# Optimization experiments

Hardware: AMD Instinct MI355X
Metric: run time of the kernel (lower is better)

The kernel has to match this reference:

```python
import jax, jax.numpy as jnp
import numpy as np

B, T, C, H = 2, 2048, 2048, 16
HD = C // H  # head dim = 128
ROPE_BASE = 10000.0


def apply_rope(x):
    # x: [B, T, H, HD]; interleaved-pair rotation as in torchtune RoPE
    t = x.shape[1]
    half = x.shape[-1] // 2
    theta = 1.0 / (ROPE_BASE ** (jnp.arange(0, HD, 2, dtype=jnp.float32) / HD))  # [HD/2]
    ang = jnp.arange(t, dtype=jnp.float32)[:, None] * theta[None, :]  # [T, HD/2]
    cos = jnp.cos(ang)[None, :, None, :]  # [1, T, 1, HD/2]
    sin = jnp.sin(ang)[None, :, None, :]
    xs = x.reshape(*x.shape[:-1], half, 2)  # [B,T,H,HD/2,2]
    x0, x1 = xs[..., 0], xs[..., 1]
    out = jnp.stack([x0 * cos - x1 * sin, x1 * cos + x0 * sin], axis=-1)
    return out.reshape(x.shape)


def setup_inputs() -> dict:
    key = jax.random.key(0)
    k1, k2, k3 = jax.random.split(key, 3)
    x = jax.random.normal(k1, (B, T, C), dtype=jnp.float32)
    attn_mask = jnp.tril(jnp.ones((T, T), dtype=bool))[None, None]  # causal [1,1,T,T]
    W_attn = jax.random.normal(k2, (3 * C, C), dtype=jnp.float32) * (C ** -0.5)
    W_proj = jax.random.normal(k3, (C, C), dtype=jnp.float32) * (C ** -0.5)
    return {"x": x, "attn_mask": attn_mask, "W_attn": W_attn, "W_proj": W_proj}


def reference(x, attn_mask, W_attn, W_proj):
    b, t, c = x.shape
    qkv = x @ W_attn.T  # [B,T,3C]
    q, k, v = jnp.split(qkv, 3, axis=-1)
    q = apply_rope(q.reshape(b, t, H, HD)).transpose(0, 2, 1, 3)  # [B,H,T,HD]
    k = apply_rope(k.reshape(b, t, H, HD)).transpose(0, 2, 1, 3)
    v = v.reshape(b, t, H, HD).transpose(0, 2, 1, 3)
    scale = 1.0 / jnp.sqrt(jnp.float32(HD))
    scores = jnp.einsum("bhqd,bhkd->bhqk", q, k) * scale
    scores = jnp.where(attn_mask, scores, jnp.finfo(scores.dtype).min)
    probs = jax.nn.softmax(scores, axis=-1)
    y = jnp.einsum("bhqk,bhkd->bhqd", probs, v)  # [B,H,T,HD]
    y = y.transpose(0, 2, 1, 3).reshape(b, t, c)
    return y @ W_proj.T
```

## Files before the change

### kernel.cpp

```cpp
#include <hip/hip_runtime.h>
#include <hip/hip_bf16.h>
#include <math.h>

typedef unsigned short u16;
typedef unsigned int   u32;
typedef __attribute__((ext_vector_type(8)))  short bf16x8;
typedef __attribute__((ext_vector_type(4)))  float f32x4;
typedef __attribute__((ext_vector_type(16))) float f32x16;

#define B_  2
#define T_  2048
#define C_  2048
#define H_  16
#define HD_ 128
#define M_  4096
#define N3C 6144

__device__ __forceinline__ float bf2f_lo(u32 u) { return __uint_as_float(u << 16); }
__device__ __forceinline__ float bf2f_hi(u32 u) { return __uint_as_float(u & 0xffff0000u); }

__device__ __forceinline__ u16 f2bf(float f) {
    u32 u = __float_as_uint(f);
    return (u16)((u + 0x7fffu + ((u >> 16) & 1u)) >> 16);
}
__device__ __forceinline__ u32 pack2(float a, float b) {
    return (u32)f2bf(a) | ((u32)f2bf(b) << 16);
}
__device__ __forceinline__ void store1(float* p, float v) { *p = v; }
__device__ __forceinline__ void store1(__hip_bfloat16* p, float v) { *(u16*)p = f2bf(v); }

__device__ __forceinline__ void gload16(const void* g, void* l) {
    __builtin_amdgcn_global_load_lds((__attribute__((address_space(1))) void*)g,
                                     (__attribute__((address_space(3))) void*)l, 16, 0, 0);
}

__global__ __launch_bounds__(256) void cvt_bf16(const float* __restrict__ in,
                                                u16* __restrict__ out, int n8) {
    const int i = blockIdx.x * 256 + threadIdx.x;
    if (i < n8) {
        const float4 a = ((const float4*)in)[2 * i];
        const float4 b = ((const float4*)in)[2 * i + 1];
        ((uint4*)out)[i] = make_uint4(pack2(a.x, a.y), pack2(a.z, a.w),
                                      pack2(b.x, b.y), pack2(b.z, b.w));
    }
}

template <typename TO>
__global__ __launch_bounds__(256, 3) void gemm_pipe(const __hip_bfloat16* __restrict__ A,
                                                    const __hip_bfloat16* __restrict__ W,
                                                    TO* __restrict__ Cout,
                                                    int N, int K, int gx) {
    __shared__ u16 As[3][128 * 32];
    __shared__ u16 Bs[3][128 * 32];
    const int nwg = gridDim.x * gridDim.y;
    const int id  = blockIdx.y * gx + blockIdx.x;
    const int swz = (id & 7) * (nwg >> 3) + (id >> 3);
    const int bm  = (swz / gx) * 128;
    const int bn  = (swz % gx) * 128;

    const int tid  = threadIdx.x;
    const int w    = tid >> 6;
    const int lane = tid & 63;
    const int g    = lane >> 4;
    const int c    = lane & 15;
    const int wr   = (w >> 1) * 64;
    const int wc   = (w & 1) * 64;

    const int srow = lane >> 2;
    const int scol = (lane & 3) * 8;
    const __hip_bfloat16* ga0 = A + (size_t)(bm + w * 32 + srow) * K + scol;
    const __hip_bfloat16* ga1 = ga0 + (size_t)16 * K;
    const __hip_bfloat16* gb0 = W + (size_t)(bn + w * 32 + srow) * K + scol;
    const __hip_bfloat16* gb1 = gb0 + (size_t)16 * K;

#define STAGE_(bi, kk) do {                                   \
        gload16(ga0 + (kk), &As[bi][w * 1024]);               \
        gload16(ga1 + (kk), &As[bi][w * 1024 + 512]);         \
        gload16(gb0 + (kk), &Bs[bi][w * 1024]);               \
        gload16(gb1 + (kk), &Bs[bi][w * 1024 + 512]);         \
    } while (0)

    f32x4 acc[4][4];
#pragma unroll
    for (int mi = 0; mi < 4; ++mi)
#pragma unroll
        for (int ni = 0; ni < 4; ++ni)
            acc[mi][ni] = (f32x4){0.f, 0.f, 0.f, 0.f};

    const int NT = K / 32;
    STAGE_(0, 0);
    STAGE_(1, 32);

    int cur = 0;
    for (int t = 0; t < NT; ++t) {
        if (t + 1 < NT) { asm volatile("s_waitcnt vmcnt(4)" ::: "memory"); }
        else            { asm volatile("s_waitcnt vmcnt(0)" ::: "memory"); }
        __builtin_amdgcn_sched_barrier(0);
        __builtin_amdgcn_s_barrier();
        __builtin_amdgcn_sched_barrier(0);

        if (t + 2 < NT) {
            const int nb = (cur + 2 >= 3) ? cur - 1 : cur + 2;
            STAGE_(nb, (t + 2) * 32);
        }

        bf16x8 af[4], bfr[4];
#pragma unroll
        for (int mi = 0; mi < 4; ++mi)
            af[mi] = *(const bf16x8*)&As[cur][(wr + mi * 16 + c) * 32 + g * 8];
#pragma unroll
        for (int ni = 0; ni < 4; ++ni)
            bfr[ni] = *(const bf16x8*)&Bs[cur][(wc + ni * 16 + c) * 32 + g * 8];

        __builtin_amdgcn_s_setprio(1);
#pragma unroll
        for (int mi = 0; mi < 4; ++mi)
#pragma unroll
            for (int ni = 0; ni < 4; ++ni)
                acc[mi][ni] = __builtin_amdgcn_mfma_f32_16x16x32_bf16(
                    af[mi], bfr[ni], acc[mi][ni], 0, 0, 0);
        __builtin_amdgcn_s_setprio(0);

        cur = (cur + 1 == 3) ? 0 : cur + 1;
    }
#undef STAGE_

#pragma unroll
    for (int mi = 0; mi < 4; ++mi)
#pragma unroll
        for (int ni = 0; ni < 4; ++ni)
#pragma unroll
            for (int i = 0; i < 4; ++i) {
                const int row = bm + wr + mi * 16 + 4 * g + i;
                const int col = bn + wc + ni * 16 + c;
                store1(Cout + (size_t)row * N + col, acc[mi][ni][i]);
            }
}

__device__ __forceinline__ void stage_tile(u16* dst, const float* src, int ldk, int tid) {
    const int r0  = tid >> 3;
    const int off = (tid & 7) * 4;
#pragma unroll
    for (int it = 0; it < 4; ++it) {
        const int row = r0 + it * 32;
        const float4 v = *(const float4*)(src + (size_t)row * ldk + off);
        *(uint2*)&dst[row * 40 + off] = make_uint2(pack2(v.x, v.y), pack2(v.z, v.w));
    }
}
__device__ __forceinline__ void stage_tile(u16* dst, const __hip_bfloat16* src, int ldk, int tid) {
    const int r0  = tid >> 2;
    const int off = (tid & 3) * 8;
#pragma unroll
    for (int it = 0; it < 2; ++it) {
        const int row = r0 + it * 64;
        *(uint4*)&dst[row * 40 + off] = *(const uint4*)(src + (size_t)row * ldk + off);
    }
}

template <typename TA, typename TW, typename TO>
__global__ __launch_bounds__(256) void gemm_mfma(const TA* __restrict__ A,
                                                 const TW* __restrict__ W,
                                                 TO* __restrict__ Cout,
                                                 int N, int K, int gx) {
    __shared__ u16 As[128 * 40];
    __shared__ u16 Bs[128 * 40];
    const int nwg = gridDim.x * gridDim.y;
    const int id  = blockIdx.y * gx + blockIdx.x;
    const int swz = (id & 7) * (nwg >> 3) + (id >> 3);
    const int bm  = (swz / gx) * 128;
    const int bn  = (swz % gx) * 128;

    const int tid  = threadIdx.x;
    const int w    = tid >> 6;
    const int lane = tid & 63;
    const int g    = lane >> 4;
    const int c    = lane & 15;
    const int wr   = (w >> 1) * 64;
    const int wc   = (w & 1) * 64;

    f32x4 acc[4][4];
#pragma unroll
    for (int mi = 0; mi < 4; ++mi)
#pragma unroll
        for (int ni = 0; ni < 4; ++ni)
            acc[mi][ni] = (f32x4){0.f, 0.f, 0.f, 0.f};

    const TA* Ab = A + (size_t)bm * K;
    const TW* Wb = W + (size_t)bn * K;

    for (int k0 = 0; k0 < K; k0 += 32) {
        __syncthreads();
        stage_tile(As, Ab + k0, K, tid);
        stage_tile(Bs, Wb + k0, K, tid);
        __syncthreads();

        bf16x8 af[4], bfr[4];
#pragma unroll
        for (int mi = 0; mi < 4; ++mi)
            af[mi] = *(const bf16x8*)&As[(wr + mi * 16 + c) * 40 + g * 8];
#pragma unroll
        for (int ni = 0; ni < 4; ++ni)
            bfr[ni] = *(const bf16x8*)&Bs[(wc + ni * 16 + c) * 40 + g * 8];
#pragma unroll
        for (int mi = 0; mi < 4; ++mi)
#pragma unroll
            for (int ni = 0; ni < 4; ++ni)
                acc[mi][ni] = __builtin_amdgcn_mfma_f32_16x16x32_bf16(
                    af[mi], bfr[ni], acc[mi][ni], 0, 0, 0);
    }

#pragma unroll
    for (int mi = 0; mi < 4; ++mi)
#pragma unroll
        for (int ni = 0; ni < 4; ++ni)
#pragma unroll
            for (int i = 0; i < 4; ++i) {
                const int row = bm + wr + mi * 16 + 4 * g + i;
                const int col = bn + wc + ni * 16 + c;
                store1(Cout + (size_t)row * N + col, acc[mi][ni][i]);
            }
}

__global__ __launch_bounds__(256) void rope_kernel(__hip_bfloat16* __restrict__ qkv) {
    const int id  = blockIdx.x * 256 + threadIdx.x;
    const int i   = id & 63;
    const int h   = (id >> 6) & (H_ - 1);
    const int qk  = (id >> 10) & 1;
    const int row = id >> 11;
    const int t   = row & (T_ - 1);
    const size_t base = (size_t)row * N3C + (size_t)qk * C_ + h * HD_ + 2 * i;
    u32* p = (u32*)((u16*)qkv + base);
    const u32 v = *p;
    const float x0 = bf2f_lo(v), x1 = bf2f_hi(v);
    const float l2th = 0.20762050593046f;
    const float theta = exp2f(-(float)i * l2th);
    const float ang = (float)t * theta;
    float s, cc;
    sincosf(ang, &s, &cc);
    *p = pack2(x0 * cc - x1 * s, x1 * cc + x0 * s);
}

__device__ __forceinline__ int PI_(int s) {
    return (s & 51) | ((s & 4) << 1) | ((s & 8) >> 1);
}

__global__ __launch_bounds__(256, 2) void attn_mfma2(const __hip_bfloat16* __restrict__ qkv,
                                                     __hip_bfloat16* __restrict__ y) {
    __shared__ u16 Ks[64 * 136];
    __shared__ u16 Vt[128 * 72];
    __shared__ float Red[128];

    const int tid  = threadIdx.x;
    const int w    = tid >> 6;
    const int lane = tid & 63;
    const int c31  = lane & 31;
    const int hi   = lane >> 5;
    const int bid  = blockIdx.x;
    const int bh   = bid & 31;
    const int qb   = 15 - (bid >> 5);
    const int b    = bh >> 4, h = bh & 15;
    const int q0   = qb * 128;

    const size_t base = (size_t)b * T_ * N3C + (size_t)h * HD_;
    const __hip_bfloat16* Qp = qkv + base;
    const __hip_bfloat16* Kp = qkv + base + C_;
    const __hip_bfloat16* Vp = qkv + base + 2 * C_;

    bf16x8 qf[8];
    {
        const size_t qoff = (size_t)(q0 + w * 32 + c31) * N3C + hi * 8;
#pragma unroll
        for (int kc = 0; kc < 8; ++kc)
            qf[kc] = *(const bf16x8*)(Qp + qoff + kc * 16);
    }

    f32x16 o[4];
#pragma unroll
    for (int db = 0; db < 4; ++db)
#pragma unroll
        for (int r = 0; r < 16; ++r) o[db][r] = 0.f;

    float m_ = -1e30f, l_ = 0.f;
    const int   myq   = q0 + w * 32 + c31;
    const float SCALE = 0.08838834764831845f;

    const int s_   = tid >> 2;
    const int dsub = tid & 3;
    const int vcol = PI_(s_) ^ (dsub << 4);

    uint4 kreg[4], vreg[4];
#pragma unroll
    for (int it = 0; it < 4; ++it) {
        const int col = dsub * 32 + it * 8;
        const size_t goff = (size_t)s_ * N3C + col;
        kreg[it] = *(const uint4*)(Kp + goff);
        vreg[it] = *(const uint4*)(Vp + goff);
    }

    const int nkt = 2 * qb + 2;
    for (int kt = 0; kt < nkt; ++kt) {
        __syncthreads();
#pragma unroll
        for (int it = 0; it < 4; ++it) {
            const int col = dsub * 32 + it * 8;
            *(uint4*)&Ks[s_ * 136 + col] = kreg[it];
            const u32 vw[4] = {vreg[it].x, vreg[it].y, vreg[it].z, vreg[it].w};
#pragma unroll
            for (int j = 0; j < 8; ++j)
                Vt[(col + j) * 72 + vcol] = (u16)(vw[j >> 1] >> ((j & 1) * 16));
        }
        if (kt + 1 < nkt) {
#pragma unroll
            for (int it = 0; it < 4; ++it) {
                const int col = dsub * 32 + it * 8;
                const size_t goff = (size_t)((kt + 1) * 64 + s_) * N3C + col;
                kreg[it] = *(const uint4*)(Kp + goff);
                vreg[it] = *(const uint4*)(Vp + goff);
            }
        }
        __syncthreads();

        const int k0 = kt * 64;
        f32x16 sA, sB;
#pragma unroll
        for (int r = 0; r < 16; ++r) { sA[r] = 0.f; sB[r] = 0.f; }
        __builtin_amdgcn_s_setprio(1);
#pragma unroll
        for (int kc = 0; kc < 8; ++kc) {
            const bf16x8 ka = *(const bf16x8*)&Ks[c31 * 136 + kc * 16 + hi * 8];
            sA = __builtin_amdgcn_mfma_f32_32x32x16_bf16(ka, qf[kc], sA, 0, 0, 0);
            const bf16x8 kb_ = *(const bf16x8*)&Ks[(32 + c31) * 136 + kc * 16 + hi * 8];
            sB = __builtin_amdgcn_mfma_f32_32x32x16_bf16(kb_, qf[kc], sB, 0, 0, 0);
        }
        __builtin_amdgcn_s_setprio(0);

        float pmax = -1e30f;
#pragma unroll
        for (int r = 0; r < 16; ++r) {
            const int cr = (r & 3) + 8 * (r >> 2) + 4 * hi;
            sA[r] = (k0 + cr      <= myq) ? sA[r] * SCALE : -1e30f;
            sB[r] = (k0 + 32 + cr <= myq) ? sB[r] * SCALE : -1e30f;
            pmax = fmaxf(pmax, fmaxf(sA[r], sB[r]));
        }
        pmax = fmaxf(pmax, __shfl_xor(pmax, 32));

        if (__any(pmax > m_ + 8.f)) {
            const float mn   = fmaxf(m_, pmax);
            const float corr = __expf(m_ - mn);
            Red[w * 32 + c31] = corr;
            float cf[16];
#pragma unroll
            for (int r = 0; r < 16; ++r)
                cf[r] = Red[w * 32 + ((r & 3) + 8 * (r >> 2) + 4 * hi)];
#pragma unroll
            for (int db = 0; db < 4; ++db)
#pragma unroll
                for (int r = 0; r < 16; ++r) o[db][r] *= cf[r];
            l_ *= corr;
            m_ = mn;
        }

        float psum = 0.f;
#pragma unroll
        for (int r = 0; r < 16; ++r) {
            sA[r] = __expf(sA[r] - m_); psum += sA[r];
            sB[r] = __expf(sB[r] - m_); psum += sB[r];
        }
        psum += __shfl_xor(psum, 32);
        l_ += psum;

        __builtin_amdgcn_s_setprio(1);
#pragma unroll
        for (int kb2 = 0; kb2 < 2; ++kb2) {
#pragma unroll
            for (int c2 = 0; c2 < 2; ++c2) {
                union { u32 u[4]; bf16x8 v; } pk;
#pragma unroll
                for (int q2 = 0; q2 < 4; ++q2) {
                    const int r = 8 * c2 + 2 * q2;
                    const float e0 = kb2 ? sB[r]     : sA[r];
                    const float e1 = kb2 ? sB[r + 1] : sA[r + 1];
                    pk.u[q2] = pack2(e0, e1);
                }
#pragma unroll
                for (int db = 0; db < 4; ++db) {
                    const int colb = (kb2 * 32 + c2 * 16 + hi * 8) ^ (db << 4);
                    const bf16x8 vb = *(const bf16x8*)&Vt[(db * 32 + c31) * 72 + colb];
                    o[db] = __builtin_amdgcn_mfma_f32_32x32x16_bf16(pk.v, vb, o[db], 0, 0, 0);
                }
            }
        }
        __builtin_amdgcn_s_setprio(0);
    }

    Red[w * 32 + c31] = l_;
    float lv[16];
#pragma unroll
    for (int r = 0; r < 16; ++r)
        lv[r] = 1.f / Red[w * 32 + ((r & 3) + 8 * (r >> 2) + 4 * hi)];
#pragma unroll
    for (int db = 0; db < 4; ++db)
#pragma unroll
        for (int r = 0; r < 16; ++r) {
            const int q = q0 + w * 32 + (r & 3) + 8 * (r >> 2) + 4 * hi;
            store1(y + (size_t)(b * T_ + q) * C_ + h * HD_ + db * 32 + c31,
                   o[db][r] * lv[r]);
        }
}

extern "C" void kernel_launch(void* const* d_in, const int* in_sizes, int n_in,
                              void* d_out, int out_size, void* d_ws, size_t ws_size,
                              hipStream_t stream) {
    const float* x  = (const float*)d_in[0];
    const float* Wa = (const float*)d_in[2];
    const float* Wp = (const float*)d_in[3];
    float* out = (float*)d_out;

    u16* ws = (u16*)d_ws;
    __hip_bfloat16* qkv = (__hip_bfloat16*)ws;
    __hip_bfloat16* y   = (__hip_bfloat16*)(ws + (size_t)M_ * N3C);

    const size_t NEED = ((size_t)M_ * N3C + (size_t)M_ * C_ +
                         (size_t)M_ * C_ +
                         (size_t)N3C * C_ + (size_t)C_ * C_) * 2;

    if (ws_size >= NEED) {
        u16* xb  = ws + (size_t)M_ * N3C + (size_t)M_ * C_;
        u16* Wab = xb + (size_t)M_ * C_;
        u16* Wpb = Wab + (size_t)N3C * C_;

        cvt_bf16<<<(M_ * C_ / 8 + 255) / 256, 256, 0, stream>>>(x, xb, M_ * C_ / 8);
        cvt_bf16<<<(N3C * C_ / 8 + 255) / 256, 256, 0, stream>>>(Wa, Wab, N3C * C_ / 8);
        cvt_bf16<<<(C_ * C_ / 8 + 255) / 256, 256, 0, stream>>>(Wp, Wpb, C_ * C_ / 8);

        gemm_pipe<__hip_bfloat16>
            <<<dim3(N3C / 128, M_ / 128), 256, 0, stream>>>(
                (const __hip_bfloat16*)xb, (const __hip_bfloat16*)Wab, qkv, N3C, C_, N3C / 128);
        rope_kernel<<<(M_ * C_) / 256, 256, 0, stream>>>(qkv);
        attn_mfma2<<<512, 256, 0, stream>>>(qkv, y);
        gemm_pipe<float>
            <<<dim3(C_ / 128, M_ / 128), 256, 0, stream>>>(
                y, (const __hip_bfloat16*)Wpb, out, C_, C_, C_ / 128);
    } else {
        gemm_mfma<float, float, __hip_bfloat16>
            <<<dim3(N3C / 128, M_ / 128), 256, 0, stream>>>(x, Wa, qkv, N3C, C_, N3C / 128);
        rope_kernel<<<(M_ * C_) / 256, 256, 0, stream>>>(qkv);
        attn_mfma2<<<512, 256, 0, stream>>>(qkv, y);
        gemm_mfma<__hip_bfloat16, float, float>
            <<<dim3(C_ / 128, M_ / 128), 256, 0, stream>>>(y, Wp, out, C_, C_, C_ / 128);
    }
}
```

Measured before the change: 307.3 us.

## Fuse RoPE into QKV GEMM epilogue, swizzle LDS tiles, reorder attention blocks

Applies the rotary embedding inside the QKV GEMM epilogue: each lane computes its angle with sincosf and gets its pair partner through a lane shuffle. This removes the separate rope_kernel launch and its full read-write pass over Q and K. It also XOR-swizzles the LDS staging columns in gemm_pipe to reduce bank conflicts on fragment reads, and changes the attention block-to-query-tile mapping so the second half of the grid visits tiles in ascending order for load balance. The extra sincosf calls in the epilogue add compute to the GEMM.

After: 352.5 us. 1.15x slower.

```diff
diff --git a/kernel.cpp b/kernel.cpp
--- a/kernel.cpp
+++ b/kernel.cpp
@@ -45,7 +45,7 @@
     }
 }
 
-template <typename TO>
+template <typename TO, bool ROPE>
 __global__ __launch_bounds__(256, 3) void gemm_pipe(const __hip_bfloat16* __restrict__ A,
                                                     const __hip_bfloat16* __restrict__ W,
                                                     TO* __restrict__ Cout,
@@ -67,7 +67,7 @@
     const int wc   = (w & 1) * 64;
 
     const int srow = lane >> 2;
-    const int scol = (lane & 3) * 8;
+    const int scol = (((lane & 3) ^ ((lane >> 2) & 3))) * 8;
     const __hip_bfloat16* ga0 = A + (size_t)(bm + w * 32 + srow) * K + scol;
     const __hip_bfloat16* ga1 = ga0 + (size_t)16 * K;
     const __hip_bfloat16* gb0 = W + (size_t)(bn + w * 32 + srow) * K + scol;
@@ -90,6 +90,8 @@
     const int NT = K / 32;
     STAGE_(0, 0);
     STAGE_(1, 32);
+
+    const int gsw = (g ^ (c & 3)) * 8;
 
     int cur = 0;
     for (int t = 0; t < NT; ++t) {
@@ -107,10 +109,10 @@
         bf16x8 af[4], bfr[4];
 #pragma unroll
         for (int mi = 0; mi < 4; ++mi)
-            af[mi] = *(const bf16x8*)&As[cur][(wr + mi * 16 + c) * 32 + g * 8];
-#pragma unroll
-        for (int ni = 0; ni < 4; ++ni)
-            bfr[ni] = *(const bf16x8*)&Bs[cur][(wc + ni * 16 + c) * 32 + g * 8];
+            af[mi] = *(const bf16x8*)&As[cur][(wr + mi * 16 + c) * 32 + gsw];
+#pragma unroll
+        for (int ni = 0; ni < 4; ++ni)
+            bfr[ni] = *(const bf16x8*)&Bs[cur][(wc + ni * 16 + c) * 32 + gsw];
 
         __builtin_amdgcn_s_setprio(1);
 #pragma unroll
@@ -124,6 +126,26 @@
         cur = (cur + 1 == 3) ? 0 : cur + 1;
     }
 #undef STAGE_
+
+    if (ROPE && bn < 2 * C_) {
+#pragma unroll
+        for (int ni = 0; ni < 4; ++ni) {
+            const int ip = ((wc + ni * 16 + c) >> 1) & 63;
+            const float theta = exp2f(-(float)ip * 0.20762050593046f);
+            const float sgn = (c & 1) ? 1.f : -1.f;
+#pragma unroll
+            for (int mi = 0; mi < 4; ++mi)
+#pragma unroll
+                for (int i = 0; i < 4; ++i) {
+                    const int row = bm + wr + mi * 16 + 4 * g + i;
+                    float s, co;
+                    sincosf((float)(row & (T_ - 1)) * theta, &s, &co);
+                    const float own = acc[mi][ni][i];
+                    const float par = __shfl_xor(own, 1);
+                    acc[mi][ni][i] = own * co + sgn * par * s;
+                }
+        }
+    }
 
 #pragma unroll
     for (int mi = 0; mi < 4; ++mi)
@@ -257,7 +279,7 @@
     const int hi   = lane >> 5;
     const int bid  = blockIdx.x;
     const int bh   = bid & 31;
-    const int qb   = 15 - (bid >> 5);
+    const int qb   = (bid < 256) ? 15 - (bid >> 5) : (bid >> 5) - 8;
     const int b    = bh >> 4, h = bh & 15;
     const int q0   = qb * 128;
 
@@ -433,12 +455,11 @@
         cvt_bf16<<<(N3C * C_ / 8 + 255) / 256, 256, 0, stream>>>(Wa, Wab, N3C * C_ / 8);
         cvt_bf16<<<(C_ * C_ / 8 + 255) / 256, 256, 0, stream>>>(Wp, Wpb, C_ * C_ / 8);
 
-        gemm_pipe<__hip_bfloat16>
+        gemm_pipe<__hip_bfloat16, true>
             <<<dim3(N3C / 128, M_ / 128), 256, 0, stream>>>(
                 (const __hip_bfloat16*)xb, (const __hip_bfloat16*)Wab, qkv, N3C, C_, N3C / 128);
-        rope_kernel<<<(M_ * C_) / 256, 256, 0, stream>>>(qkv);
         attn_mfma2<<<512, 256, 0, stream>>>(qkv, y);
-        gemm_pipe<float>
+        gemm_pipe<float, false>
             <<<dim3(C_ / 128, M_ / 128), 256, 0, stream>>>(
                 y, (const __hip_bfloat16*)Wpb, out, C_, C_, C_ / 128);
     } else {
```

## Fuse bf16 conversions, rebalance attention block order, shuffle-transpose V into LDS

Applied to the files above, without the earlier changes.

Merges the three fp32-to-bf16 conversion launches into a single kernel that picks its source by global index, removing two launches. Changes the attention query-block ordering so the second half of the grid runs short causal blocks in ascending order, aiming for better load balance. Replaces the scalar 16-bit scatter that transposes V into LDS with cross-lane shuffles that pack pairs and write 8-byte chunks, cutting LDS store instructions at the cost of extra shuffle and select work.

After: 311.8 us. About the same (+1.5%).

```diff
diff --git a/kernel.cpp b/kernel.cpp
--- a/kernel.cpp
+++ b/kernel.cpp
@@ -34,15 +34,23 @@
                                      (__attribute__((address_space(3))) void*)l, 16, 0, 0);
 }
 
-__global__ __launch_bounds__(256) void cvt_bf16(const float* __restrict__ in,
-                                                u16* __restrict__ out, int n8) {
+__global__ __launch_bounds__(256) void cvt_all(const float* __restrict__ x,
+                                               const float* __restrict__ Wa,
+                                               const float* __restrict__ Wp,
+                                               u16* __restrict__ xb,
+                                               u16* __restrict__ Wab,
+                                               u16* __restrict__ Wpb) {
+    const int n_x  = M_ * C_ / 8;
+    const int n_wa = N3C * C_ / 8;
     const int i = blockIdx.x * 256 + threadIdx.x;
-    if (i < n8) {
-        const float4 a = ((const float4*)in)[2 * i];
-        const float4 b = ((const float4*)in)[2 * i + 1];
-        ((uint4*)out)[i] = make_uint4(pack2(a.x, a.y), pack2(a.z, a.w),
-                                      pack2(b.x, b.y), pack2(b.z, b.w));
-    }
+    const float* src; u16* dst; int j;
+    if (i < n_x)            { src = x;  dst = xb;  j = i; }
+    else if (i < n_x + n_wa){ src = Wa; dst = Wab; j = i - n_x; }
+    else                    { src = Wp; dst = Wpb; j = i - n_x - n_wa; }
+    const float4 a = ((const float4*)src)[2 * j];
+    const float4 b = ((const float4*)src)[2 * j + 1];
+    ((uint4*)dst)[j] = make_uint4(pack2(a.x, a.y), pack2(a.z, a.w),
+                                  pack2(b.x, b.y), pack2(b.z, b.w));
 }
 
 template <typename TO>
@@ -257,7 +265,7 @@
     const int hi   = lane >> 5;
     const int bid  = blockIdx.x;
     const int bh   = bid & 31;
-    const int qb   = 15 - (bid >> 5);
+    const int qb   = (bid < 256) ? 15 - (bid >> 5) : (bid >> 5) - 8;
     const int b    = bh >> 4, h = bh & 15;
     const int q0   = qb * 128;
 
@@ -286,7 +294,10 @@
 
     const int s_   = tid >> 2;
     const int dsub = tid & 3;
-    const int vcol = PI_(s_) ^ (dsub << 4);
+    const int b0   = s_ & 1;
+    const int b1   = (s_ >> 1) & 1;
+    const int pc   = PI_(s_ & 60) ^ (dsub << 4);
+    const int dbase = dsub * 32 + (s_ & 3) * 8;
 
     uint4 kreg[4], vreg[4];
 #pragma unroll
@@ -301,14 +312,45 @@
     for (int kt = 0; kt < nkt; ++kt) {
         __syncthreads();
 #pragma unroll
-        for (int it = 0; it < 4; ++it) {
-            const int col = dsub * 32 + it * 8;
-            *(uint4*)&Ks[s_ * 136 + col] = kreg[it];
-            const u32 vw[4] = {vreg[it].x, vreg[it].y, vreg[it].z, vreg[it].w};
-#pragma unroll
-            for (int j = 0; j < 8; ++j)
-                Vt[(col + j) * 72 + vcol] = (u16)(vw[j >> 1] >> ((j & 1) * 16));
-        }
+        for (int it = 0; it < 4; ++it)
+            *(uint4*)&Ks[s_ * 136 + dsub * 32 + it * 8] = kreg[it];
+
+        {
+            uint4 s1a = b0 ? vreg[0] : vreg[1];
+            uint4 s1b = b0 ? vreg[2] : vreg[3];
+            uint4 r1a, r1b;
+            r1a.x = __shfl_xor(s1a.x, 4); r1a.y = __shfl_xor(s1a.y, 4);
+            r1a.z = __shfl_xor(s1a.z, 4); r1a.w = __shfl_xor(s1a.w, 4);
+            r1b.x = __shfl_xor(s1b.x, 4); r1b.y = __shfl_xor(s1b.y, 4);
+            r1b.z = __shfl_xor(s1b.z, 4); r1b.w = __shfl_xor(s1b.w, 4);
+            const uint4 ownA = b0 ? vreg[1] : vreg[0];
+            const uint4 ownB = b0 ? vreg[3] : vreg[2];
+            const uint4 eA = b0 ? r1a : ownA, oA = b0 ? ownA : r1a;
+            const uint4 eB = b0 ? r1b : ownB, oB = b0 ? ownB : r1b;
+            u32 pA[8], pB[8];
+#pragma unroll
+            for (int wd = 0; wd < 4; ++wd) {
+                const u32 ew = ((const u32*)&eA)[wd], ow = ((const u32*)&oA)[wd];
+                pA[2 * wd]     = (ew & 0xffffu) | (ow << 16);
+                pA[2 * wd + 1] = (ew >> 16)     | (ow & 0xffff0000u);
+                const u32 ew2 = ((const u32*)&eB)[wd], ow2 = ((const u32*)&oB)[wd];
+                pB[2 * wd]     = (ew2 & 0xffffu) | (ow2 << 16);
+                pB[2 * wd + 1] = (ew2 >> 16)     | (ow2 & 0xffff0000u);
+            }
+            u32 keep[8], recv[8];
+#pragma unroll
+            for (int s = 0; s < 8; ++s) {
+                keep[s] = b1 ? pB[s] : pA[s];
+                recv[s] = __shfl_xor(b1 ? pA[s] : pB[s], 8);
+            }
+#pragma unroll
+            for (int s = 0; s < 8; ++s) {
+                const u32 lo = b1 ? recv[s] : keep[s];
+                const u32 hi2 = b1 ? keep[s] : recv[s];
+                *(uint2*)&Vt[(dbase + s) * 72 + pc] = make_uint2(lo, hi2);
+            }
+        }
+
         if (kt + 1 < nkt) {
 #pragma unroll
             for (int it = 0; it < 4; ++it) {
@@ -429,9 +471,8 @@
         u16* Wab = xb + (size_t)M_ * C_;
         u16* Wpb = Wab + (size_t)N3C * C_;
 
-        cvt_bf16<<<(M_ * C_ / 8 + 255) / 256, 256, 0, stream>>>(x, xb, M_ * C_ / 8);
-        cvt_bf16<<<(N3C * C_ / 8 + 255) / 256, 256, 0, stream>>>(Wa, Wab, N3C * C_ / 8);
-        cvt_bf16<<<(C_ * C_ / 8 + 255) / 256, 256, 0, stream>>>(Wp, Wpb, C_ * C_ / 8);
+        const int n8_total = (M_ * C_ + N3C * C_ + C_ * C_) / 8;
+        cvt_all<<<n8_total / 256, 256, 0, stream>>>(x, Wa, Wp, xb, Wab, Wpb);
 
         gemm_pipe<__hip_bfloat16>
             <<<dim3(N3C / 128, M_ / 128), 256, 0, stream>>>(
```
